# Optimization experiments

Hardware: AMD Instinct MI355X
Metric: run time of the kernel (lower is better)

Reference implementation:

```python
import jax, jax.numpy as jnp
import numpy as np

B, S, HID = 2, 2048, 2048
NH, NKV, D = 16, 8, 128
N_REP = NH // NKV
EPS = 1e-6
THETA = 10000.0


def setup_inputs() -> dict:
    key = jax.random.key(0)
    ks = jax.random.split(key, 6)
    s = 0.02
    return {
        "hidden_states": jax.random.normal(ks[0], (B, S, HID), jnp.float32),
        "attention_mask": jnp.ones((B, S), jnp.float32),
        "wq": jax.random.normal(ks[1], (HID, NH * D), jnp.float32) * s,
        "wk": jax.random.normal(ks[2], (HID, NKV * D), jnp.float32) * s,
        "wv": jax.random.normal(ks[3], (HID, NKV * D), jnp.float32) * s,
        "wo": jax.random.normal(ks[4], (NH * D, HID), jnp.float32) * s,
        "q_norm_w": jnp.ones((D,), jnp.float32),
        "k_norm_w": jnp.ones((D,), jnp.float32),
    }


def _rms_norm(x, w, eps=EPS):
    # x: (..., D); computed in fp32 like the torch module
    x32 = x.astype(jnp.float32)
    var = jnp.mean(x32 * x32, axis=-1, keepdims=True)
    return (w * (x32 * jax.lax.rsqrt(var + eps))).astype(x.dtype)


def _rotate_half(x):
    x1, x2 = jnp.split(x, 2, axis=-1)
    return jnp.concatenate((-x2, x1), axis=-1)


def _rope_cos_sin(seq_len, dim, dtype):
    inv_freq = 1.0 / (THETA ** (jnp.arange(0, dim, 2, dtype=jnp.float32) / dim))
    t = jnp.arange(seq_len, dtype=jnp.float32)
    freqs = t[:, None] * inv_freq[None, :]          # (S, D/2)
    emb = jnp.concatenate((freqs, freqs), axis=-1)  # (S, D)
    # broadcast to (1, 1, S, D)
    return jnp.cos(emb).astype(dtype)[None, None], jnp.sin(emb).astype(dtype)[None, None]


def reference(hidden_states, attention_mask, wq, wk, wv, wo, q_norm_w, k_norm_w):
    b, s, _ = hidden_states.shape
    # QKV projections (bias-free)
    q = (hidden_states @ wq).reshape(b, s, NH, D).transpose(0, 2, 1, 3)   # (b, nh, s, d)
    k = (hidden_states @ wk).reshape(b, s, NKV, D).transpose(0, 2, 1, 3)  # (b, nkv, s, d)
    v = (hidden_states @ wv).reshape(b, s, NKV, D).transpose(0, 2, 1, 3)
    # per-head QK RMSNorm
    q = _rms_norm(q, q_norm_w)
    k = _rms_norm(k, k_norm_w)
    # RoPE
    cos, sin = _rope_cos_sin(s, D, q.dtype)
    q = q * cos + _rotate_half(q) * sin
    k = k * cos + _rotate_half(k) * sin
    # GQA repeat kv heads
    k = jnp.repeat(k, N_REP, axis=1)
    v = jnp.repeat(v, N_REP, axis=1)
    # SDPA (bidirectional, additive padding mask)
    scale = 1.0 / np.sqrt(D)
    scores = jnp.einsum("bhqd,bhkd->bhqk", q, k) * scale
    add_mask = (1.0 - attention_mask)[:, None, None, :] * jnp.finfo(scores.dtype).min
    scores = scores + add_mask
    attn = jax.nn.softmax(scores, axis=-1)
    out = jnp.einsum("bhqk,bhkd->bhqd", attn, v)
    out = out.transpose(0, 2, 1, 3).reshape(b, s, NH * D)
    return out @ wo
```

## Files before the change

kernel.cpp:

```cpp
#include <hip/hip_runtime.h>
#include <stdint.h>

#define BB   2
#define SS   2048
#define HID  2048
#define NHQ  16
#define NKV  8
#define DD   128
#define QKVW 4096

typedef __bf16 v8bf   __attribute__((ext_vector_type(8)));
typedef float  f32x4  __attribute__((ext_vector_type(4)));
typedef float  f32x16 __attribute__((ext_vector_type(16)));

__device__ __forceinline__ float bf2f(ushort u) {
    union { unsigned int i; float f; } x; x.i = ((unsigned int)u) << 16; return x.f;
}
__device__ __forceinline__ ushort f2bf(float f) {
    union { float f; unsigned int i; } x; x.f = f;
    unsigned int i = x.i;
    return (ushort)((i + 0x7fffu + ((i >> 16) & 1u)) >> 16);
}
__device__ __forceinline__ v8bf as_bf8(uint4 u) { return __builtin_bit_cast(v8bf, u); }

__device__ __forceinline__ unsigned int cvtpk_bf16(float lo, float hi) {
    unsigned int r;
    asm("v_cvt_pk_bf16_f32 %0, %1, %2" : "=v"(r) : "v"(lo), "v"(hi));
    return r;
}

__device__ __forceinline__ void store_el(float* p, float v)  { *p = v; }
__device__ __forceinline__ void store_el(ushort* p, float v) { *p = f2bf(v); }

__device__ __forceinline__ void gll16(const ushort* g, ushort* l) {
    __builtin_amdgcn_global_load_lds(
        (const __attribute__((address_space(1))) void*)g,
        (__attribute__((address_space(3))) void*)l, 16, 0, 0);
}

__device__ __forceinline__ int swz_off(int r, int lcolb) {
    return r * 64 + (((lcolb) ^ ((r & 4) << 3)) >> 1);
}

#define PREP_CAST   8192
#define PREP_WQ     (PREP_CAST)
#define PREP_WK     (PREP_WQ + 4096)
#define PREP_WV     (PREP_WK + 2048)
#define PREP_WO     (PREP_WV + 2048)
#define PREP_TOTAL  (PREP_WO + 4096)

__device__ __forceinline__ void tcast_body(
    const float* __restrict__ in, ushort* __restrict__ out,
    int K, int N, int bx, int by, int t)
{
    __shared__ float tile[32][33];
    int n0 = bx * 32, k0 = by * 32;
    int tx = t & 31, ty = t >> 5;
#pragma unroll
    for (int i = 0; i < 32; i += 8)
        tile[ty + i][tx] = in[(size_t)(k0 + ty + i) * N + n0 + tx];
    __syncthreads();
#pragma unroll
    for (int i = 0; i < 32; i += 8)
        out[(size_t)(n0 + ty + i) * K + k0 + tx] = f2bf(tile[tx][ty + i]);
}

__global__ __launch_bounds__(256) void prep(
    const float* __restrict__ X,  const float* __restrict__ wq,
    const float* __restrict__ wk, const float* __restrict__ wv,
    const float* __restrict__ wo,
    ushort* __restrict__ Xb, ushort* __restrict__ WqkvT, ushort* __restrict__ Wot)
{
    int bid = blockIdx.x, t = threadIdx.x;
    if (bid < PREP_CAST) {
        int i = (bid * 256 + t) * 4;
        float4 v = *(const float4*)&X[i];
        ushort4 o = { f2bf(v.x), f2bf(v.y), f2bf(v.z), f2bf(v.w) };
        *(ushort4*)&Xb[i] = o;
    } else if (bid < PREP_WK) {
        int l = bid - PREP_WQ;
        tcast_body(wq, WqkvT, 2048, 2048, l & 63, l >> 6, t);
    } else if (bid < PREP_WV) {
        int l = bid - PREP_WK;
        tcast_body(wk, WqkvT + (size_t)2048 * 2048, 2048, 1024, l & 31, l >> 5, t);
    } else if (bid < PREP_WO) {
        int l = bid - PREP_WV;
        tcast_body(wv, WqkvT + (size_t)3072 * 2048, 2048, 1024, l & 31, l >> 5, t);
    } else {
        int l = bid - PREP_WO;
        tcast_body(wo, Wot, 2048, 2048, l & 63, l >> 6, t);
    }
}

template <typename OutT>
__global__ __launch_bounds__(512, 2) void gemm_bt2(
    const ushort* __restrict__ A, const ushort* __restrict__ Bt,
    OutT* __restrict__ C, int M, int N, int K)
{
    __shared__ __align__(16) ushort As[3][256 * 64];
    __shared__ __align__(16) ushort Bs[3][128 * 64];
    const int t = threadIdx.x;
    const int lane = t & 63, wave = t >> 6;
    const int quad = lane >> 4, l15 = lane & 15;
    const int m0 = blockIdx.y * 256, n0 = blockIdx.x * 128;
    const int wm = (wave >> 1) * 64;
    const int wn = (wave & 1) * 64;

    const f32x4 zv = {0.f, 0.f, 0.f, 0.f};
    f32x4 acc[4][4];
#pragma unroll
    for (int i = 0; i < 4; i++)
#pragma unroll
        for (int j = 0; j < 4; j++) acc[i][j] = zv;

    int arow[4], acol[4];
#pragma unroll
    for (int j = 0; j < 4; j++) {
        int p = (j * 512 + t) * 16;
        int l = p ^ (((p >> 9) & 1) << 5);
        arow[j] = l >> 7; acol[j] = (l & 127) >> 1;
    }
    int brow[2], bcol[2];
#pragma unroll
    for (int j = 0; j < 2; j++) {
        int p = (j * 512 + t) * 16;
        int l = p ^ (((p >> 9) & 1) << 5);
        brow[j] = l >> 7; bcol[j] = (l & 127) >> 1;
    }

    int aoff[4][2], boff[2][2][2];
#pragma unroll
    for (int mf = 0; mf < 4; mf++)
#pragma unroll
        for (int kk = 0; kk < 2; kk++)
            aoff[mf][kk] = swz_off(wm + mf * 16 + l15, kk * 64 + quad * 16);
#pragma unroll
    for (int q = 0; q < 2; q++)
#pragma unroll
        for (int nf = 0; nf < 2; nf++)
#pragma unroll
            for (int kk = 0; kk < 2; kk++)
                boff[q][nf][kk] = swz_off(wn + q * 32 + nf * 16 + l15, kk * 64 + quad * 16);

#define STAGE_A(j, slot, kk0) \
    gll16(&A[(size_t)(m0 + arow[j]) * K + (kk0) + acol[j]], &As[slot][0] + ((j) * 512 + t) * 8)
#define STAGE_B(j, slot, kk0) \
    gll16(&Bt[(size_t)(n0 + brow[j]) * K + (kk0) + bcol[j]], &Bs[slot][0] + ((j) * 512 + t) * 8)

    const int NT = K >> 6;

#pragma unroll
    for (int j = 0; j < 4; j++) STAGE_A(j, 0, 0);
#pragma unroll
    for (int j = 0; j < 2; j++) STAGE_B(j, 0, 0);
#pragma unroll
    for (int j = 0; j < 4; j++) STAGE_A(j, 1, 64);
#pragma unroll
    for (int j = 0; j < 2; j++) STAGE_B(j, 1, 64);
    asm volatile("s_waitcnt vmcnt(6)" ::: "memory");
    __builtin_amdgcn_s_barrier();

    int cur = 0;
    for (int T = 0; T < NT; T++) {
        const ushort* Ac = &As[cur][0];
        const ushort* Bc = &Bs[cur][0];
        int stg = cur + 2; if (stg >= 3) stg -= 3;
        const int k2 = (T + 2) << 6;
        const bool do_stage = (T + 2) < NT;

        uint4 af[4][2], bf[2][2];
#pragma unroll
        for (int mf = 0; mf < 4; mf++)
#pragma unroll
            for (int kk = 0; kk < 2; kk++)
                af[mf][kk] = *(const uint4*)&Ac[aoff[mf][kk]];
#pragma unroll
        for (int nf = 0; nf < 2; nf++)
#pragma unroll
            for (int kk = 0; kk < 2; kk++)
                bf[nf][kk] = *(const uint4*)&Bc[boff[0][nf][kk]];
        if (do_stage) {
            STAGE_A(0, stg, k2); STAGE_A(1, stg, k2); STAGE_B(0, stg, k2);
        }
        __builtin_amdgcn_s_barrier();
        asm volatile("s_waitcnt lgkmcnt(0)" ::: "memory");
        __builtin_amdgcn_sched_barrier(0);
        __builtin_amdgcn_s_setprio(1);
#pragma unroll
        for (int mf = 0; mf < 4; mf++)
#pragma unroll
            for (int nf = 0; nf < 2; nf++)
#pragma unroll
                for (int kk = 0; kk < 2; kk++)
                    acc[mf][nf] = __builtin_amdgcn_mfma_f32_16x16x32_bf16(
                        as_bf8(af[mf][kk]), as_bf8(bf[nf][kk]), acc[mf][nf], 0, 0, 0);
        __builtin_amdgcn_s_setprio(0);
        __builtin_amdgcn_s_barrier();

#pragma unroll
        for (int nf = 0; nf < 2; nf++)
#pragma unroll
            for (int kk = 0; kk < 2; kk++)
                bf[nf][kk] = *(const uint4*)&Bc[boff[1][nf][kk]];
        if (do_stage) {
            STAGE_A(2, stg, k2); STAGE_A(3, stg, k2); STAGE_B(1, stg, k2);
            asm volatile("s_waitcnt vmcnt(6)" ::: "memory");
        } else if (T + 2 == NT) {
            asm volatile("s_waitcnt vmcnt(0)" ::: "memory");
        }
        __builtin_amdgcn_s_barrier();
        asm volatile("s_waitcnt lgkmcnt(0)" ::: "memory");
        __builtin_amdgcn_sched_barrier(0);
        __builtin_amdgcn_s_setprio(1);
#pragma unroll
        for (int mf = 0; mf < 4; mf++)
#pragma unroll
            for (int nf = 0; nf < 2; nf++)
#pragma unroll
                for (int kk = 0; kk < 2; kk++)
                    acc[mf][2 + nf] = __builtin_amdgcn_mfma_f32_16x16x32_bf16(
                        as_bf8(af[mf][kk]), as_bf8(bf[nf][kk]), acc[mf][2 + nf], 0, 0, 0);
        __builtin_amdgcn_s_setprio(0);
        __builtin_amdgcn_s_barrier();

        cur++; if (cur == 3) cur = 0;
    }
#undef STAGE_A
#undef STAGE_B

#pragma unroll
    for (int mf = 0; mf < 4; mf++)
#pragma unroll
        for (int nf = 0; nf < 4; nf++)
#pragma unroll
            for (int r = 0; r < 4; r++) {
                int row = m0 + wm + mf * 16 + quad * 4 + r;
                int col = n0 + wn + nf * 16 + l15;
                store_el(&C[(size_t)row * N + col], acc[mf][nf][r]);
            }
}

__global__ __launch_bounds__(256) void norm_rope(
    ushort* __restrict__ qkv, const float* __restrict__ qw, const float* __restrict__ kw)
{
    int row = blockIdx.x;
    int s = row & (SS - 1);
    int lane = threadIdx.x & 63, wave = threadIdx.x >> 6;
    int l = lane & 31, hsel = lane >> 5;
    float d0 = (float)(2 * l), d1 = d0 + 1.0f;
    float inv0 = expf(-d0 * (1.0f / 64.0f) * 9.210340371976184f);
    float inv1 = expf(-d1 * (1.0f / 64.0f) * 9.210340371976184f);
    float c0, s0, c1, s1;
    sincosf((float)s * inv0, &s0, &c0);
    sincosf((float)s * inv1, &s1, &c1);
    float qw0 = qw[2 * l], qw1 = qw[2 * l + 1], qy0 = qw[2 * l + 64], qy1 = qw[2 * l + 65];
    float kw0 = kw[2 * l], kw1 = kw[2 * l + 1], ky0 = kw[2 * l + 64], ky1 = kw[2 * l + 65];

#pragma unroll
    for (int pass = 0; pass < 3; pass++) {
        int h = pass * 8 + wave * 2 + hsel;
        ushort* p = qkv + (size_t)row * QKVW + h * 128;
        unsigned int ulo = *(const unsigned int*)&p[2 * l];
        unsigned int uhi = *(const unsigned int*)&p[2 * l + 64];
        float x0 = bf2f((ushort)ulo), x1 = bf2f((ushort)(ulo >> 16));
        float y0 = bf2f((ushort)uhi), y1 = bf2f((ushort)(uhi >> 16));
        float ssum = x0 * x0 + x1 * x1 + y0 * y0 + y1 * y1;
#pragma unroll
        for (int xm = 1; xm < 32; xm <<= 1) ssum += __shfl_xor(ssum, xm, 64);
        float r = rsqrtf(ssum * (1.0f / 128.0f) + 1e-6f);
        bool isq = (h < 16);
        float w0 = isq ? qw0 : kw0, w1 = isq ? qw1 : kw1;
        float v0 = isq ? qy0 : ky0, v1 = isq ? qy1 : ky1;
        float sc = isq ? (0.08838834764831845f * 1.4426950408889634f) : 1.0f;
        float nx0 = w0 * (x0 * r), nx1 = w1 * (x1 * r);
        float ny0 = v0 * (y0 * r), ny1 = v1 * (y1 * r);
        float ox0 = (nx0 * c0 - ny0 * s0) * sc, ox1 = (nx1 * c1 - ny1 * s1) * sc;
        float oy0 = (ny0 * c0 + nx0 * s0) * sc, oy1 = (ny1 * c1 + nx1 * s1) * sc;
        *(unsigned int*)&p[2 * l]      = (unsigned int)f2bf(ox0) | ((unsigned int)f2bf(ox1) << 16);
        *(unsigned int*)&p[2 * l + 64] = (unsigned int)f2bf(oy0) | ((unsigned int)f2bf(oy1) << 16);
    }
}

__global__ __launch_bounds__(256, 2) void flash_attn(
    const ushort* __restrict__ qkv, const float* __restrict__ mask, ushort* __restrict__ O)
{
    __shared__ __align__(16) ushort Ks[2][64 * 128];
    __shared__ __align__(16) ushort Vt[128 * 64];
    __shared__ __align__(16) float  Madd[SS];
    const int t = threadIdx.x;
    const int lane = t & 63, wave = t >> 6;
    const int l31 = lane & 31, half = lane >> 5;
    const int b = blockIdx.z, h = blockIdx.y, q0 = blockIdx.x * 128;
    const int kh = h >> 1;

#pragma unroll
    for (int i = 0; i < 2; i++) {
        int idx = i * 1024 + t * 4;
        float4 mv = *(const float4*)&mask[b * SS + idx];
        float4 o = { (1.f - mv.x) * -1e30f, (1.f - mv.y) * -1e30f,
                     (1.f - mv.z) * -1e30f, (1.f - mv.w) * -1e30f };
        *(float4*)&Madd[idx] = o;
    }

    uint4 aq[8];
    {
        const ushort* qp = qkv + ((size_t)(b * SS + q0 + wave * 32 + l31)) * QKVW + h * 128 + half * 8;
#pragma unroll
        for (int kt = 0; kt < 8; kt++) aq[kt] = *(const uint4*)&qp[kt * 16];
    }
    f32x16 acc_o[4];
#pragma unroll
    for (int i = 0; i < 4; i++)
#pragma unroll
        for (int r = 0; r < 16; r++) acc_o[i][r] = 0.f;
    float lp[4] = {0.f, 0.f, 0.f, 0.f};

    const ushort* Kg = qkv + (size_t)b * SS * QKVW + 2048 + kh * 128;
    const ushort* Vg = qkv + (size_t)b * SS * QKVW + 3072 + kh * 128;

    const int vp = t & 31, vdc = t >> 5;
    uint4 vreg[4];
#define LOAD_V(K0)                                                                  \
    {                                                                               \
        _Pragma("unroll")                                                           \
        for (int pass = 0; pass < 2; pass++) {                                      \
            int d0 = (vdc + pass * 8) * 8;                                          \
            vreg[pass * 2 + 0] = *(const uint4*)&Vg[(size_t)((K0) + 2 * vp) * QKVW + d0];     \
            vreg[pass * 2 + 1] = *(const uint4*)&Vg[(size_t)((K0) + 2 * vp + 1) * QKVW + d0]; \
        }                                                                           \
    }
#define STAGE_K(K0, buf)                                                            \
    {                                                                               \
        _Pragma("unroll")                                                           \
        for (int i = 0; i < 4; i++) {                                               \
            int chunk = i * 256 + t;                                                \
            int row = chunk >> 4, cp = chunk & 15;                                  \
            int cl = cp ^ (row & 15);                                               \
            gll16(&Kg[(size_t)((K0) + row) * QKVW + cl * 8], &Ks[buf][chunk * 8]);  \
        }                                                                           \
    }

    STAGE_K(0, 0);
    LOAD_V(0);

    for (int k0 = 0; k0 < SS; k0 += 64) {
        const int cur = (k0 >> 6) & 1;
        __syncthreads();
        if (k0 + 64 < SS) STAGE_K(k0 + 64, cur ^ 1);
#pragma unroll
        for (int pass = 0; pass < 2; pass++) {
            const ushort* pa_ = (const ushort*)&vreg[pass * 2 + 0];
            const ushort* pb_ = (const ushort*)&vreg[pass * 2 + 1];
            int d0 = (vdc + pass * 8) * 8;
#pragma unroll
            for (int j = 0; j < 8; j++) {
                int cp = (vp >> 2) ^ j;
                unsigned int v = (unsigned int)pa_[j] | ((unsigned int)pb_[j] << 16);
                *(unsigned int*)&Vt[(d0 + j) * 64 + cp * 8 + (vp & 3) * 2] = v;
            }
        }
        if (k0 + 64 < SS) LOAD_V(k0 + 64);
        asm volatile("s_waitcnt lgkmcnt(0)" ::: "memory");
        __builtin_amdgcn_sched_barrier(0);
        __builtin_amdgcn_s_barrier();

        f32x16 sc[2];
#pragma unroll
        for (int nt = 0; nt < 2; nt++)
#pragma unroll
            for (int g = 0; g < 4; g++) {
                f32x4 em = *(const f32x4*)&Madd[k0 + nt * 32 + 4 * half + g * 8];
#pragma unroll
                for (int j = 0; j < 4; j++) sc[nt][g * 4 + j] = em[j];
            }
        __builtin_amdgcn_s_setprio(1);
#pragma unroll
        for (int nt = 0; nt < 2; nt++) {
#pragma unroll
            for (int kt = 0; kt < 8; kt++) {
                int cp = (kt * 2 + half) ^ (l31 & 15);
                uint4 bk = *(const uint4*)&Ks[cur][(nt * 32 + l31) * 128 + cp * 8];
                sc[nt] = __builtin_amdgcn_mfma_f32_32x32x16_bf16(
                    as_bf8(bk), as_bf8(aq[kt]), sc[nt], 0, 0, 0);
            }
        }
        __builtin_amdgcn_s_setprio(0);

        uint4 pa[4];
#pragma unroll
        for (int nt = 0; nt < 2; nt++) {
            float p[16];
#pragma unroll
            for (int r = 0; r < 16; r++) {
                float pv = __builtin_amdgcn_exp2f(sc[nt][r]);
                p[r] = pv;
                lp[r & 3] += pv;
            }
            unsigned int pk[8];
#pragma unroll
            for (int i = 0; i < 8; i++) pk[i] = cvtpk_bf16(p[2 * i], p[2 * i + 1]);
            auto sA = __builtin_amdgcn_permlane32_swap(pk[0], pk[2], false, false);
            auto sB = __builtin_amdgcn_permlane32_swap(pk[1], pk[3], false, false);
            auto sC = __builtin_amdgcn_permlane32_swap(pk[4], pk[6], false, false);
            auto sD = __builtin_amdgcn_permlane32_swap(pk[5], pk[7], false, false);
            uint4 f0, f1;
            f0.x = sA[0]; f0.y = sB[0]; f0.z = sA[1]; f0.w = sB[1];
            f1.x = sC[0]; f1.y = sD[0]; f1.z = sC[1]; f1.w = sD[1];
            pa[nt * 2 + 0] = f0;
            pa[nt * 2 + 1] = f1;
        }

        __builtin_amdgcn_s_setprio(1);
#pragma unroll
        for (int kt2 = 0; kt2 < 4; kt2++) {
            int kc = kt2 * 2 + half;
            int co = (kc ^ (l31 & 7)) * 8;
#pragma unroll
            for (int nt = 0; nt < 4; nt++) {
                uint4 bv = *(const uint4*)&Vt[(nt * 32 + l31) * 64 + co];
                acc_o[nt] = __builtin_amdgcn_mfma_f32_32x32x16_bf16(
                    as_bf8(pa[kt2]), as_bf8(bv), acc_o[nt], 0, 0, 0);
            }
        }
        __builtin_amdgcn_s_setprio(0);
    }
    float lsum = (lp[0] + lp[1]) + (lp[2] + lp[3]);
    lsum += __shfl_xor(lsum, 32, 64);
    float linv = 1.0f / lsum;
    float li[16];
#pragma unroll
    for (int r = 0; r < 16; r++)
        li[r] = __shfl(linv, (r & 3) + 8 * (r >> 2) + 4 * half, 64);
#pragma unroll
    for (int nt = 0; nt < 4; nt++)
#pragma unroll
        for (int r = 0; r < 16; r++) {
            int prow = (r & 3) + 8 * (r >> 2) + 4 * half;
            int qrow = q0 + wave * 32 + prow;
            int d = nt * 32 + l31;
            float v = acc_o[nt][r] * li[r];
            O[((size_t)(b * SS + qrow)) * (NHQ * DD) + h * 128 + d] = f2bf(v);
        }
}

extern "C" void kernel_launch(void* const* d_in, const int* in_sizes, int n_in,
                              void* d_out, int out_size, void* d_ws, size_t ws_size,
                              hipStream_t stream)
{
    const float* X    = (const float*)d_in[0];
    const float* mask = (const float*)d_in[1];
    const float* wq   = (const float*)d_in[2];
    const float* wk   = (const float*)d_in[3];
    const float* wv   = (const float*)d_in[4];
    const float* wo   = (const float*)d_in[5];
    const float* qnw  = (const float*)d_in[6];
    const float* knw  = (const float*)d_in[7];
    float* out = (float*)d_out;

    const size_t M = (size_t)BB * SS;
    ushort* Xb    = (ushort*)d_ws;
    ushort* WqkvT = Xb    + M * HID;
    ushort* Wot   = WqkvT + (size_t)4096 * HID;
    ushort* QKV   = Wot   + (size_t)2048 * 2048;
    ushort* Obuf  = QKV   + M * QKVW;

    prep<<<PREP_TOTAL, 256, 0, stream>>>(X, wq, wk, wv, wo, Xb, WqkvT, Wot);

    gemm_bt2<ushort><<<dim3(4096 / 128, 4096 / 256), 512, 0, stream>>>(Xb, WqkvT, QKV, 4096, 4096, 2048);

    norm_rope<<<(int)M, 256, 0, stream>>>(QKV, qnw, knw);

    flash_attn<<<dim3(SS / 128, NHQ, BB), 256, 0, stream>>>(QKV, mask, Obuf);

    gemm_bt2<float><<<dim3(2048 / 128, 4096 / 256), 512, 0, stream>>>(Obuf, Wot, out, 4096, 2048, 2048);
}
```

Before: 345.0 us.

## Process two 32-row query groups per wave in flash attention for K/V reuse

Each wave now handles 64 query rows (two 32-row groups) instead of 32, so a block covers 256 queries and the grid along the sequence is halved. Each K and V fragment read from LDS feeds two MFMAs, halving K/V staging and LDS traffic per query. In exchange, register use roughly doubles for accumulators, Q fragments and scores, so launch bounds drop to one block per CU target. The grid shrinks to 256 blocks, which lowers occupancy and latency hiding.

```diff
diff --git a/kernel.cpp b/kernel.cpp
--- a/kernel.cpp
+++ b/kernel.cpp
@@ -281,7 +281,7 @@
     }
 }
 
-__global__ __launch_bounds__(256, 2) void flash_attn(
+__global__ __launch_bounds__(256, 1) void flash_attn(
     const ushort* __restrict__ qkv, const float* __restrict__ mask, ushort* __restrict__ O)
 {
     __shared__ __align__(16) ushort Ks[2][64 * 128];
@@ -290,7 +290,7 @@
     const int t = threadIdx.x;
     const int lane = t & 63, wave = t >> 6;
     const int l31 = lane & 31, half = lane >> 5;
-    const int b = blockIdx.z, h = blockIdx.y, q0 = blockIdx.x * 128;
+    const int b = blockIdx.z, h = blockIdx.y, q0 = blockIdx.x * 256;
     const int kh = h >> 1;
 
 #pragma unroll
@@ -302,18 +302,26 @@
         *(float4*)&Madd[idx] = o;
     }
 
-    uint4 aq[8];
-    {
-        const ushort* qp = qkv + ((size_t)(b * SS + q0 + wave * 32 + l31)) * QKVW + h * 128 + half * 8;
-#pragma unroll
-        for (int kt = 0; kt < 8; kt++) aq[kt] = *(const uint4*)&qp[kt * 16];
-    }
-    f32x16 acc_o[4];
-#pragma unroll
-    for (int i = 0; i < 4; i++)
-#pragma unroll
-        for (int r = 0; r < 16; r++) acc_o[i][r] = 0.f;
-    float lp[4] = {0.f, 0.f, 0.f, 0.f};
+    uint4 aq[2][8];
+#pragma unroll
+    for (int g = 0; g < 2; g++) {
+        const ushort* qp = qkv + ((size_t)(b * SS + q0 + wave * 64 + g * 32 + l31)) * QKVW
+                         + h * 128 + half * 8;
+#pragma unroll
+        for (int kt = 0; kt < 8; kt++) aq[g][kt] = *(const uint4*)&qp[kt * 16];
+    }
+    f32x16 acc_o[2][4];
+#pragma unroll
+    for (int g = 0; g < 2; g++)
+#pragma unroll
+        for (int i = 0; i < 4; i++)
+#pragma unroll
+            for (int r = 0; r < 16; r++) acc_o[g][i][r] = 0.f;
+    float lp[2][4];
+#pragma unroll
+    for (int g = 0; g < 2; g++)
+#pragma unroll
+        for (int j = 0; j < 4; j++) lp[g][j] = 0.f;
 
     const ushort* Kg = qkv + (size_t)b * SS * QKVW + 2048 + kh * 128;
     const ushort* Vg = qkv + (size_t)b * SS * QKVW + 3072 + kh * 128;
@@ -364,14 +372,17 @@
         __builtin_amdgcn_sched_barrier(0);
         __builtin_amdgcn_s_barrier();
 
-        f32x16 sc[2];
+        f32x16 sc[2][2];
 #pragma unroll
         for (int nt = 0; nt < 2; nt++)
 #pragma unroll
-            for (int g = 0; g < 4; g++) {
-                f32x4 em = *(const f32x4*)&Madd[k0 + nt * 32 + 4 * half + g * 8];
-#pragma unroll
-                for (int j = 0; j < 4; j++) sc[nt][g * 4 + j] = em[j];
+            for (int g4 = 0; g4 < 4; g4++) {
+                f32x4 em = *(const f32x4*)&Madd[k0 + nt * 32 + 4 * half + g4 * 8];
+#pragma unroll
+                for (int j = 0; j < 4; j++) {
+                    sc[0][nt][g4 * 4 + j] = em[j];
+                    sc[1][nt][g4 * 4 + j] = em[j];
+                }
             }
         __builtin_amdgcn_s_setprio(1);
 #pragma unroll
@@ -380,35 +391,39 @@
             for (int kt = 0; kt < 8; kt++) {
                 int cp = (kt * 2 + half) ^ (l31 & 15);
                 uint4 bk = *(const uint4*)&Ks[cur][(nt * 32 + l31) * 128 + cp * 8];
-                sc[nt] = __builtin_amdgcn_mfma_f32_32x32x16_bf16(
-                    as_bf8(bk), as_bf8(aq[kt]), sc[nt], 0, 0, 0);
+                sc[0][nt] = __builtin_amdgcn_mfma_f32_32x32x16_bf16(
+                    as_bf8(bk), as_bf8(aq[0][kt]), sc[0][nt], 0, 0, 0);
+                sc[1][nt] = __builtin_amdgcn_mfma_f32_32x32x16_bf16(
+                    as_bf8(bk), as_bf8(aq[1][kt]), sc[1][nt], 0, 0, 0);
             }
         }
         __builtin_amdgcn_s_setprio(0);
 
-        uint4 pa[4];
-#pragma unroll
-        for (int nt = 0; nt < 2; nt++) {
-            float p[16];
-#pragma unroll
-            for (int r = 0; r < 16; r++) {
-                float pv = __builtin_amdgcn_exp2f(sc[nt][r]);
-                p[r] = pv;
-                lp[r & 3] += pv;
-            }
-            unsigned int pk[8];
-#pragma unroll
-            for (int i = 0; i < 8; i++) pk[i] = cvtpk_bf16(p[2 * i], p[2 * i + 1]);
-            auto sA = __builtin_amdgcn_permlane32_swap(pk[0], pk[2], false, false);
-            auto sB = __builtin_amdgcn_permlane32_swap(pk[1], pk[3], false, false);
-            auto sC = __builtin_amdgcn_permlane32_swap(pk[4], pk[6], false, false);
-            auto sD = __builtin_amdgcn_permlane32_swap(pk[5], pk[7], false, false);
-            uint4 f0, f1;
-            f0.x = sA[0]; f0.y = sB[0]; f0.z = sA[1]; f0.w = sB[1];
-            f1.x = sC[0]; f1.y = sD[0]; f1.z = sC[1]; f1.w = sD[1];
-            pa[nt * 2 + 0] = f0;
-            pa[nt * 2 + 1] = f1;
-        }
+        uint4 pa[2][4];
+#pragma unroll
+        for (int g = 0; g < 2; g++)
+#pragma unroll
+            for (int nt = 0; nt < 2; nt++) {
+                float p[16];
+#pragma unroll
+                for (int r = 0; r < 16; r++) {
+                    float pv = __builtin_amdgcn_exp2f(sc[g][nt][r]);
+                    p[r] = pv;
+                    lp[g][r & 3] += pv;
+                }
+                unsigned int pk[8];
+#pragma unroll
+                for (int i = 0; i < 8; i++) pk[i] = cvtpk_bf16(p[2 * i], p[2 * i + 1]);
+                auto sA = __builtin_amdgcn_permlane32_swap(pk[0], pk[2], false, false);
+                auto sB = __builtin_amdgcn_permlane32_swap(pk[1], pk[3], false, false);
+                auto sC = __builtin_amdgcn_permlane32_swap(pk[4], pk[6], false, false);
+                auto sD = __builtin_amdgcn_permlane32_swap(pk[5], pk[7], false, false);
+                uint4 f0, f1;
+                f0.x = sA[0]; f0.y = sB[0]; f0.z = sA[1]; f0.w = sB[1];
+                f1.x = sC[0]; f1.y = sD[0]; f1.z = sC[1]; f1.w = sD[1];
+                pa[g][nt * 2 + 0] = f0;
+                pa[g][nt * 2 + 1] = f1;
+            }
 
         __builtin_amdgcn_s_setprio(1);
 #pragma unroll
@@ -418,29 +433,35 @@
 #pragma unroll
             for (int nt = 0; nt < 4; nt++) {
                 uint4 bv = *(const uint4*)&Vt[(nt * 32 + l31) * 64 + co];
-                acc_o[nt] = __builtin_amdgcn_mfma_f32_32x32x16_bf16(
-                    as_bf8(pa[kt2]), as_bf8(bv), acc_o[nt], 0, 0, 0);
+                acc_o[0][nt] = __builtin_amdgcn_mfma_f32_32x32x16_bf16(
+                    as_bf8(pa[0][kt2]), as_bf8(bv), acc_o[0][nt], 0, 0, 0);
+                acc_o[1][nt] = __builtin_amdgcn_mfma_f32_32x32x16_bf16(
+                    as_bf8(pa[1][kt2]), as_bf8(bv), acc_o[1][nt], 0, 0, 0);
             }
         }
         __builtin_amdgcn_s_setprio(0);
     }
-    float lsum = (lp[0] + lp[1]) + (lp[2] + lp[3]);
-    lsum += __shfl_xor(lsum, 32, 64);
-    float linv = 1.0f / lsum;
-    float li[16];
-#pragma unroll
-    for (int r = 0; r < 16; r++)
-        li[r] = __shfl(linv, (r & 3) + 8 * (r >> 2) + 4 * half, 64);
-#pragma unroll
-    for (int nt = 0; nt < 4; nt++)
-#pragma unroll
-        for (int r = 0; r < 16; r++) {
-            int prow = (r & 3) + 8 * (r >> 2) + 4 * half;
-            int qrow = q0 + wave * 32 + prow;
-            int d = nt * 32 + l31;
-            float v = acc_o[nt][r] * li[r];
-            O[((size_t)(b * SS + qrow)) * (NHQ * DD) + h * 128 + d] = f2bf(v);
-        }
+
+#pragma unroll
+    for (int g = 0; g < 2; g++) {
+        float lsum = (lp[g][0] + lp[g][1]) + (lp[g][2] + lp[g][3]);
+        lsum += __shfl_xor(lsum, 32, 64);
+        float linv = 1.0f / lsum;
+        float li[16];
+#pragma unroll
+        for (int r = 0; r < 16; r++)
+            li[r] = __shfl(linv, (r & 3) + 8 * (r >> 2) + 4 * half, 64);
+#pragma unroll
+        for (int nt = 0; nt < 4; nt++)
+#pragma unroll
+            for (int r = 0; r < 16; r++) {
+                int prow = (r & 3) + 8 * (r >> 2) + 4 * half;
+                int qrow = q0 + wave * 64 + g * 32 + prow;
+                int d = nt * 32 + l31;
+                float v = acc_o[g][nt][r] * li[r];
+                O[((size_t)(b * SS + qrow)) * (NHQ * DD) + h * 128 + d] = f2bf(v);
+            }
+    }
 }
 
 extern "C" void kernel_launch(void* const* d_in, const int* in_sizes, int n_in,
@@ -470,7 +491,7 @@
 
     norm_rope<<<(int)M, 256, 0, stream>>>(QKV, qnw, knw);
 
-    flash_attn<<<dim3(SS / 128, NHQ, BB), 256, 0, stream>>>(QKV, mask, Obuf);
+    flash_attn<<<dim3(SS / 256, NHQ, BB), 256, 0, stream>>>(QKV, mask, Obuf);
 
     gemm_bt2<float><<<dim3(2048 / 128, 4096 / 256), 512, 0, stream>>>(Obuf, Wot, out, 4096, 2048, 2048);
 }
```

Result: slower. 365.7 us (+6.0%).

## Add 256x256-tile GEMM with split-K-half double buffering for QKV projection

Applied to the files above, without the earlier changes.

Adds a new bf16 GEMM kernel using 256x256 output tiles per 512-thread block (one block per CU), with each 64-wide K step staged as two 32-wide swizzled LDS halves. Global-to-LDS loads for the next step are interleaved with MFMA phases, and setprio raises wave priority around compute. It replaces the 256x128 tiled kernel for the QKV projection to raise arithmetic intensity per LDS byte and cut global traffic. The trade-off is fewer blocks (256 for 256 CUs), higher register pressure and more barriers per iteration.

```diff
diff --git a/kernel.cpp b/kernel.cpp
--- a/kernel.cpp
+++ b/kernel.cpp
@@ -40,6 +40,9 @@
 
 __device__ __forceinline__ int swz_off(int r, int lcolb) {
     return r * 64 + (((lcolb) ^ ((r & 4) << 3)) >> 1);
+}
+__device__ __forceinline__ int hswz(int r, int colb) {
+    return r * 32 + (((colb) ^ ((r & 8) << 2)) >> 1);
 }
 
 #define PREP_CAST   8192
@@ -92,6 +95,149 @@
     }
 }
 
+__global__ __launch_bounds__(512, 1) void gemm256(
+    const ushort* __restrict__ A, const ushort* __restrict__ Bt,
+    ushort* __restrict__ C, int M, int N, int K)
+{
+    __shared__ __align__(16) ushort As[2][2][256 * 32];
+    __shared__ __align__(16) ushort Bs[2][2][256 * 32];
+    const int t = threadIdx.x;
+    const int lane = t & 63, wave = t >> 6;
+    const int quad = lane >> 4, l15 = lane & 15;
+    const int m0 = blockIdx.y * 256, n0 = blockIdx.x * 256;
+    const int wm = (wave >> 1) * 64;
+    const int wn = (wave & 1) * 128;
+
+    const f32x4 zv = {0.f, 0.f, 0.f, 0.f};
+    f32x4 acc[4][8];
+#pragma unroll
+    for (int i = 0; i < 4; i++)
+#pragma unroll
+        for (int j = 0; j < 8; j++) acc[i][j] = zv;
+
+    int srow[2], scol[2];
+#pragma unroll
+    for (int j = 0; j < 2; j++) {
+        int p16 = (j * 512 + t) * 16;
+        int lg = p16 ^ (((p16 >> 9) & 1) << 5);
+        srow[j] = lg >> 6; scol[j] = (lg & 63) >> 1;
+    }
+    int aoff[4], boff[8];
+#pragma unroll
+    for (int mf = 0; mf < 4; mf++) aoff[mf] = hswz(wm + mf * 16 + l15, quad * 16);
+#pragma unroll
+    for (int nf = 0; nf < 8; nf++) boff[nf] = hswz(wn + nf * 16 + l15, quad * 16);
+
+#define STAGE_HALF(buf, hh, kb)                                                          \
+    {                                                                                    \
+        _Pragma("unroll")                                                                \
+        for (int j = 0; j < 2; j++)                                                      \
+            gll16(&A[(size_t)(m0 + srow[j]) * K + (kb) + scol[j]],                       \
+                  &As[buf][hh][(j * 512 + t) * 8]);                                      \
+        _Pragma("unroll")                                                                \
+        for (int j = 0; j < 2; j++)                                                      \
+            gll16(&Bt[(size_t)(n0 + srow[j]) * K + (kb) + scol[j]],                      \
+                  &Bs[buf][hh][(j * 512 + t) * 8]);                                      \
+    }
+
+    const int NT = K >> 6;
+
+    STAGE_HALF(0, 0, 0);
+    STAGE_HALF(0, 1, 32);
+    asm volatile("s_waitcnt vmcnt(4)" ::: "memory");
+    __builtin_amdgcn_s_barrier();
+
+    uint4 af[4], bf[4];
+    for (int T = 0; T < NT; T++) {
+        const int c = T & 1;
+        const bool stg = (T + 1) < NT;
+        const int kn = (T + 1) << 6;
+
+#pragma unroll
+        for (int mf = 0; mf < 4; mf++) af[mf] = *(const uint4*)&As[c][0][aoff[mf]];
+#pragma unroll
+        for (int nf = 0; nf < 4; nf++) bf[nf] = *(const uint4*)&Bs[c][0][boff[nf]];
+        if (stg) STAGE_HALF(c ^ 1, 0, kn);
+        __builtin_amdgcn_s_barrier();
+        asm volatile("s_waitcnt lgkmcnt(0)" ::: "memory");
+        __builtin_amdgcn_sched_barrier(0);
+        __builtin_amdgcn_s_setprio(1);
+#pragma unroll
+        for (int mf = 0; mf < 4; mf++)
+#pragma unroll
+            for (int nf = 0; nf < 4; nf++)
+                acc[mf][nf] = __builtin_amdgcn_mfma_f32_16x16x32_bf16(
+                    as_bf8(af[mf]), as_bf8(bf[nf]), acc[mf][nf], 0, 0, 0);
+        __builtin_amdgcn_s_setprio(0);
+        __builtin_amdgcn_s_barrier();
+
+#pragma unroll
+        for (int nf = 0; nf < 4; nf++) bf[nf] = *(const uint4*)&Bs[c][0][boff[4 + nf]];
+        __builtin_amdgcn_s_barrier();
+        asm volatile("s_waitcnt lgkmcnt(0)" ::: "memory");
+        __builtin_amdgcn_sched_barrier(0);
+        __builtin_amdgcn_s_setprio(1);
+#pragma unroll
+        for (int mf = 0; mf < 4; mf++)
+#pragma unroll
+            for (int nf = 0; nf < 4; nf++)
+                acc[mf][4 + nf] = __builtin_amdgcn_mfma_f32_16x16x32_bf16(
+                    as_bf8(af[mf]), as_bf8(bf[nf]), acc[mf][4 + nf], 0, 0, 0);
+        __builtin_amdgcn_s_setprio(0);
+        if (stg) asm volatile("s_waitcnt vmcnt(4)" ::: "memory");
+        else     asm volatile("s_waitcnt vmcnt(0)" ::: "memory");
+        __builtin_amdgcn_s_barrier();
+
+#pragma unroll
+        for (int mf = 0; mf < 4; mf++) af[mf] = *(const uint4*)&As[c][1][aoff[mf]];
+#pragma unroll
+        for (int nf = 0; nf < 4; nf++) bf[nf] = *(const uint4*)&Bs[c][1][boff[nf]];
+        if (stg) STAGE_HALF(c ^ 1, 1, kn + 32);
+        __builtin_amdgcn_s_barrier();
+        asm volatile("s_waitcnt lgkmcnt(0)" ::: "memory");
+        __builtin_amdgcn_sched_barrier(0);
+        __builtin_amdgcn_s_setprio(1);
+#pragma unroll
+        for (int mf = 0; mf < 4; mf++)
+#pragma unroll
+            for (int nf = 0; nf < 4; nf++)
+                acc[mf][nf] = __builtin_amdgcn_mfma_f32_16x16x32_bf16(
+                    as_bf8(af[mf]), as_bf8(bf[nf]), acc[mf][nf], 0, 0, 0);
+        __builtin_amdgcn_s_setprio(0);
+        __builtin_amdgcn_s_barrier();
+
+#pragma unroll
+        for (int nf = 0; nf < 4; nf++) bf[nf] = *(const uint4*)&Bs[c][1][boff[4 + nf]];
+        __builtin_amdgcn_s_barrier();
+        asm volatile("s_waitcnt lgkmcnt(0)" ::: "memory");
+        __builtin_amdgcn_sched_barrier(0);
+        __builtin_amdgcn_s_setprio(1);
+#pragma unroll
+        for (int mf = 0; mf < 4; mf++)
+#pragma unroll
+            for (int nf = 0; nf < 4; nf++)
+                acc[mf][4 + nf] = __builtin_amdgcn_mfma_f32_16x16x32_bf16(
+                    as_bf8(af[mf]), as_bf8(bf[nf]), acc[mf][4 + nf], 0, 0, 0);
+        __builtin_amdgcn_s_setprio(0);
+        if (stg) {
+            asm volatile("s_waitcnt vmcnt(4)" ::: "memory");
+            __builtin_amdgcn_s_barrier();
+        }
+    }
+#undef STAGE_HALF
+
+#pragma unroll
+    for (int mf = 0; mf < 4; mf++)
+#pragma unroll
+        for (int nf = 0; nf < 8; nf++)
+#pragma unroll
+            for (int r = 0; r < 4; r++) {
+                int row = m0 + wm + mf * 16 + quad * 4 + r;
+                int col = n0 + wn + nf * 16 + l15;
+                C[(size_t)row * N + col] = f2bf(acc[mf][nf][r]);
+            }
+}
+
 template <typename OutT>
 __global__ __launch_bounds__(512, 2) void gemm_bt2(
     const ushort* __restrict__ A, const ushort* __restrict__ Bt,
@@ -466,7 +612,7 @@
 
     prep<<<PREP_TOTAL, 256, 0, stream>>>(X, wq, wk, wv, wo, Xb, WqkvT, Wot);
 
-    gemm_bt2<ushort><<<dim3(4096 / 128, 4096 / 256), 512, 0, stream>>>(Xb, WqkvT, QKV, 4096, 4096, 2048);
+    gemm256<<<dim3(4096 / 256, 4096 / 256), 512, 0, stream>>>(Xb, WqkvT, QKV, 4096, 4096, 2048);
 
     norm_rope<<<(int)M, 256, 0, stream>>>(QKV, qnw, knw);
 
```

Result: no change. 340.6 us (-1.3%).
